# Kernel tuning notes

Measured on AMD Instinct MI355X. Metric: run time of the kernel, lower is better.

## Reference

```python
import jax, jax.numpy as jnp
import numpy as np

B, N, D = 16, 8192, 384   # examples, sentences per example, embedding dim
KN = 16                   # neighbors per node (kNN degree)
K, H, STEPS = 8, 128, 3   # coin dim, hidden dim, walk steps


def setup_inputs() -> dict:
    key = jax.random.key(0)
    ks = jax.random.split(key, 12)
    s = 0.02
    return {
        "sent_embs": jax.random.normal(ks[0], (B, N, D), dtype=jnp.float32),
        "q_embs": jax.random.normal(ks[1], (B, D), dtype=jnp.float32),
        "neighbors": jax.random.randint(ks[2], (B, N, KN), 0, N, dtype=jnp.int32),
        # coin_net: Linear(2D->H), ReLU, Linear(H->K)
        "coin_w1": jax.random.normal(ks[3], (2 * D, H), dtype=jnp.float32) * s,
        "coin_b1": jnp.zeros((H,), dtype=jnp.float32),
        "coin_w2": jax.random.normal(ks[4], (H, K), dtype=jnp.float32) * s,
        "coin_b2": jnp.zeros((K,), dtype=jnp.float32),
        # path_net: Linear(D+K+D->H), ReLU, Linear(H->1)
        "path_w1": jax.random.normal(ks[5], (D + K + D, H), dtype=jnp.float32) * s,
        "path_b1": jnp.zeros((H,), dtype=jnp.float32),
        "path_w2": jax.random.normal(ks[6], (H, 1), dtype=jnp.float32) * s,
        "path_b2": jnp.zeros((1,), dtype=jnp.float32),
    }


def _mlp(x, w1, b1, w2, b2):
    return jax.nn.relu(x @ w1 + b1) @ w2 + b2


def _forward(sent_embs, q_embs, neighbors,
             coin_w1, coin_b1, coin_w2, coin_b2,
             path_w1, path_b1, path_w2, path_b2):
    b, n, d = sent_embs.shape
    k = coin_w2.shape[1]
    q_bcast = jnp.broadcast_to(q_embs[:, None, :], (b, n, d))

    # coin amplitudes per node: [B, N, K]
    amps = _mlp(jnp.concatenate([sent_embs, q_bcast], axis=-1),
                coin_w1, coin_b1, coin_w2, coin_b2)

    # initial uniform walk state: 1/sqrt(N*K)
    state = jnp.full((b, n, k), 1.0 / np.sqrt(n * k), dtype=sent_embs.dtype)

    # adjacency = self-loop + edges row -> neighbors[row]; A @ X == X + masked neighbor gather-sum
    valid = (neighbors >= 0) & (neighbors < n)           # [B, N, KN]
    safe_nbrs = jnp.where(valid, neighbors, 0)
    batch_idx = jnp.arange(b)[:, None, None]

    for _ in range(STEPS):
        ns = state * amps                                # coin step
        gathered = ns[batch_idx, safe_nbrs]              # [B, N, KN, K]
        gathered = jnp.where(valid[..., None], gathered, 0.0)
        ns = ns + gathered.sum(axis=2)                   # sparse.mm(A, ns)
        norm = jnp.linalg.norm(ns.reshape(b, -1), axis=1)[:, None, None]
        state = ns / jnp.where(norm > 0, norm, 1.0)      # renormalize (guard norm==0)

    path_in = jnp.concatenate([sent_embs, state, q_bcast], axis=-1)  # [B, N, D+K+D]
    logits = _mlp(path_in, path_w1, path_b1, path_w2, path_b2)[..., 0]  # [B, N]
    return logits


def reference(sent_embs, q_embs, neighbors,
              coin_w1, coin_b1, coin_w2, coin_b2,
              path_w1, path_b1, path_w2, path_b2):
    return _forward(sent_embs, q_embs, neighbors,
                    coin_w1, coin_b1, coin_w2, coin_b2,
                    path_w1, path_b1, path_w2, path_b2)
```

## Files before the change

kernel.cpp:

```cpp
#include <hip/hip_runtime.h>

#define B_SZ 16
#define N_SZ 8192
#define D_SZ 384
#define KN_SZ 16
#define K_SZ 8
#define H_SZ 128
#define M_TOTAL (B_SZ * N_SZ)
#define KSTEPS 12
#define MT64 (M_TOTAL / 64)
#define CK 128
#define LDSB_STRIDE 144
#define HS_STRIDE 130

typedef short short8 __attribute__((ext_vector_type(8)));
typedef short short4v __attribute__((ext_vector_type(4)));
typedef float floatx4 __attribute__((ext_vector_type(4)));

__device__ __forceinline__ unsigned short f2bf(float f) {
    unsigned u = __builtin_bit_cast(unsigned, f);
    u += 0x7FFFu + ((u >> 16) & 1u);
    return (unsigned short)(u >> 16);
}
__device__ __forceinline__ float bf2f(unsigned short b) {
    unsigned u = ((unsigned)b) << 16;
    return __builtin_bit_cast(float, u);
}
__device__ __forceinline__ unsigned pkbf(float a, float b) {
    unsigned r;
    asm("v_cvt_pk_bf16_f32 %0, %1, %2" : "=v"(r) : "v"(a), "v"(b));
    return r;
}

__global__ void prep_kernel(const float* __restrict__ q_embs,
                            const float* __restrict__ coin_w1,
                            const float* __restrict__ coin_b1,
                            const float* __restrict__ path_w1,
                            const float* __restrict__ path_b1,
                            unsigned short* __restrict__ wswz,
                            float* __restrict__ qcoin, float* __restrict__ qpath,
                            float* __restrict__ norms) {
    int blk = blockIdx.x;
    int t = threadIdx.x;
    if (blk < 384) {
        int f = blk * 256 + t;
        int j  = f & 7;
        int l  = (f >> 3) & 63;
        int ss = (f >> 9) % KSTEPS;
        int ct = f / (KSTEPS * 512);
        int k = ss * 32 + ((l >> 4) << 3) + j;
        int n = ct * 16 + (l & 15);
        float v = (n < H_SZ) ? coin_w1[k * H_SZ + n]
                             : path_w1[k * H_SZ + (n - H_SZ)];
        wswz[f] = f2bf(v);
    } else if (blk == 384) {
        if (t < B_SZ) norms[t] = 0.f;
    } else {
        int b = blk - 385;
        const float* q = q_embs + b * D_SZ;
        if (t < H_SZ) {
            float acc = coin_b1[t];
            for (int d = 0; d < D_SZ; d++)
                acc += q[d] * coin_w1[(D_SZ + d) * H_SZ + t];
            qcoin[b * H_SZ + t] = acc;
        } else if (t < 2 * H_SZ) {
            int h = t - H_SZ;
            float acc = path_b1[h];
            for (int d = 0; d < D_SZ; d++)
                acc += q[d] * path_w1[(D_SZ + K_SZ + d) * H_SZ + h];
            qpath[b * H_SZ + h] = acc;
        }
    }
}

__global__ __launch_bounds__(256)
void gemm_fused(const float* __restrict__ sent,
                const unsigned short* __restrict__ wswz,
                const float* __restrict__ qcoin,
                const float* __restrict__ coin_w2,
                const float* __restrict__ coin_b2,
                unsigned short* __restrict__ hpathB,
                float* __restrict__ amps) {
    __shared__ __align__(16) short als[2 * 64 * LDSB_STRIDE];
    __shared__ float w2s[H_SZ * K_SZ];
    short* buf0 = als;
    short* buf1 = als + 64 * LDSB_STRIDE;
    const int tid = threadIdx.x;
    const int wave = tid >> 6, lane = tid & 63;
    const int m_lane = lane & 15, quad = lane >> 4;
    const int mt = blockIdx.x;
    const int b = mt >> 7;
    const float* abase = sent + (size_t)mt * 64 * D_SZ;
    const int row8 = tid >> 5;
    const int c4   = tid & 31;

    for (int i = tid; i < H_SZ * K_SZ; i += 256) w2s[i] = coin_w2[i];

    const unsigned short* wbase = wswz + (size_t)wave * 4 * KSTEPS * 512 + lane * 8;
    floatx4 acc[4][4];
#pragma unroll
    for (int rt = 0; rt < 4; rt++)
#pragma unroll
        for (int c = 0; c < 4; c++) acc[rt][c] = (floatx4){0.f, 0.f, 0.f, 0.f};

    float4 v[8];

#define STAGE_LOAD(CHUNK)                                                        \
    _Pragma("unroll")                                                            \
    for (int u = 0; u < 8; u++)                                                  \
        v[u] = *(const float4*)(abase + (size_t)(row8 + u * 8) * D_SZ +          \
                                (CHUNK) * CK + c4 * 4);

#define STAGE_STORE(BUF)                                                         \
    _Pragma("unroll")                                                            \
    for (int u = 0; u < 8; u++) {                                                \
        int2 p;                                                                  \
        p.x = (int)pkbf(v[u].x, v[u].y);                                         \
        p.y = (int)pkbf(v[u].z, v[u].w);                                         \
        *(int2*)&(BUF)[(row8 + u * 8) * LDSB_STRIDE + c4 * 4] = p;               \
    }

#define MMA_CHUNK(BUF, CHUNK)                                                    \
    _Pragma("unroll")                                                            \
    for (int sl = 0; sl < 4; sl++) {                                             \
        const int s = (CHUNK) * 4 + sl;                                          \
        short8 bfr[4];                                                           \
        _Pragma("unroll")                                                        \
        for (int cc = 0; cc < 4; cc++)                                           \
            bfr[cc] = *(const short8*)(wbase + (size_t)(cc * KSTEPS + s) * 512); \
        short8 af[4];                                                            \
        _Pragma("unroll")                                                        \
        for (int rt = 0; rt < 4; rt++)                                           \
            af[rt] = *(const short8*)&(BUF)[(rt * 16 + m_lane) * LDSB_STRIDE +   \
                                            sl * 32 + quad * 8];                 \
        _Pragma("unroll")                                                        \
        for (int rt = 0; rt < 4; rt++)                                           \
            _Pragma("unroll")                                                    \
            for (int cc = 0; cc < 4; cc++)                                       \
                acc[rt][cc] = __builtin_amdgcn_mfma_f32_16x16x32_bf16(           \
                    af[rt], bfr[cc], acc[rt][cc], 0, 0, 0);                      \
    }

    STAGE_LOAD(0);
    STAGE_STORE(buf0);
    __syncthreads();
    STAGE_LOAD(1);
    MMA_CHUNK(buf0, 0);
    STAGE_STORE(buf1);
    __syncthreads();
    STAGE_LOAD(2);
    MMA_CHUNK(buf1, 1);
    STAGE_STORE(buf0);
    __syncthreads();
    MMA_CHUNK(buf0, 2);

    if (wave >= 2) {
        const int colw = (wave & 1) * 64;
#pragma unroll
        for (int rt = 0; rt < 4; rt++) {
            int mt16 = mt * 4 + rt;
#pragma unroll
            for (int c = 0; c < 4; c++) {
                int col = colw + c * 16 + m_lane;
                int2 p;
                p.x = (int)pkbf(acc[rt][c][0], acc[rt][c][1]);
                p.y = (int)pkbf(acc[rt][c][2], acc[rt][c][3]);
                *(int2*)(hpathB + (size_t)mt16 * 2048 + col * 16 + quad * 4) = p;
            }
        }
    }
    __syncthreads();

    float* hs = (float*)als;
    if (wave < 2) {
        const int colw = wave * 64;
        float qc[4];
#pragma unroll
        for (int c = 0; c < 4; c++)
            qc[c] = qcoin[b * H_SZ + colw + c * 16 + m_lane];
#pragma unroll
        for (int rt = 0; rt < 4; rt++)
#pragma unroll
            for (int c = 0; c < 4; c++) {
                int colj = colw + c * 16 + m_lane;
#pragma unroll
                for (int j = 0; j < 4; j++) {
                    int row = rt * 16 + quad * 4 + j;
                    float hv = acc[rt][c][j] + qc[c];
                    hs[row * HS_STRIDE + colj] = hv > 0.f ? hv : 0.f;
                }
            }
    }
    __syncthreads();

    {
        const int r = tid >> 2;
        const int kk = (tid & 3) * 2;
        float a0 = coin_b2[kk], a1 = coin_b2[kk + 1];
#pragma unroll 8
        for (int c = 0; c < H_SZ; c++) {
            float hv = hs[r * HS_STRIDE + c];
            float2 w = *(const float2*)&w2s[c * 8 + kk];
            a0 += hv * w.x; a1 += hv * w.y;
        }
        const size_t m = (size_t)mt * 64 + r;
        *(float2*)(amps + m * 8 + kk) = make_float2(a0, a1);
    }
#undef STAGE_LOAD
#undef STAGE_STORE
#undef MMA_CHUNK
}

__global__ __launch_bounds__(1024)
void walk_fused(const float* __restrict__ amps,
                const int* __restrict__ neighbors,
                float* __restrict__ zfinal,
                float* __restrict__ norms) {
    __shared__ float z0buf[N_SZ];
    __shared__ float z1buf[N_SZ];
    __shared__ float bsum;
    const int tid = threadIdx.x;
    const int b = blockIdx.x >> 3;
    const int k = blockIdx.x & 7;
    const size_t nodebase = (size_t)b * N_SZ;

    float a[8];
#pragma unroll
    for (int u = 0; u < 8; u++) {
        int n = u * 1024 + tid;
        a[u] = amps[(nodebase + n) * 8 + k];
        z0buf[n] = a[u] * (1.0f / 256.0f);
    }
    if (tid == 0) bsum = 0.f;
    __syncthreads();

    float* zc = z0buf;
    float* zn = z1buf;
    float ss = 0.f;
#pragma unroll
    for (int step = 0; step < 3; step++) {
#pragma unroll
        for (int u = 0; u < 8; u++) {
            const int n = u * 1024 + tid;
            const int4* nb4 = (const int4*)(neighbors + (nodebase + n) * KN_SZ);
            int4 q0 = nb4[0], q1 = nb4[1], q2 = nb4[2], q3 = nb4[3];
            float v = zc[n];
            int idx[16] = {q0.x, q0.y, q0.z, q0.w, q1.x, q1.y, q1.z, q1.w,
                           q2.x, q2.y, q2.z, q2.w, q3.x, q3.y, q3.z, q3.w};
#pragma unroll
            for (int i = 0; i < 16; i++) {
                int nn = idx[i];
                if ((unsigned)nn < (unsigned)N_SZ) v += zc[nn];
            }
            if (step < 2) v *= a[u];
            zn[n] = v;
            if (step == 2) ss += v * v;
        }
        __syncthreads();
        float* t = zc; zc = zn; zn = t;
    }

#pragma unroll
    for (int o = 32; o > 0; o >>= 1) ss += __shfl_down(ss, o);
    if ((tid & 63) == 0) atomicAdd(&bsum, ss);
    __syncthreads();
    if (tid == 0) atomicAdd(&norms[b], bsum);

#pragma unroll
    for (int u = 0; u < 8; u++) {
        int n = u * 1024 + tid;
        zfinal[(nodebase + n) * 8 + k] = zc[n];
    }
}

__global__ __launch_bounds__(256)
void logits_kernel(const unsigned short* __restrict__ hpathB,
                   const float* __restrict__ qpath,
                   const float* __restrict__ u2,
                   const float* __restrict__ norms,
                   const float* __restrict__ path_w1,
                   const float* __restrict__ path_w2,
                   const float* __restrict__ path_b2,
                   float* __restrict__ out) {
    __shared__ float w1t[4 * 260];
    __shared__ float w2sp[4 * 33];
    __shared__ float qps[4 * 33];
    const int tid = threadIdx.x;
    const int mbase = blockIdx.x * 64;
    const int b = mbase >> 13;
    for (int i2 = tid; i2 < H_SZ * K_SZ; i2 += 256) {
        int h = i2 >> 3, j = i2 & 7;
        w1t[(h >> 5) * 260 + (h & 31) * 8 + j] = path_w1[(D_SZ + j) * H_SZ + h];
    }
    if (tid < H_SZ) {
        int idx = (tid >> 5) * 33 + (tid & 31);
        w2sp[idx] = path_w2[tid];
        qps[idx]  = qpath[b * H_SZ + tid];
    }
    __syncthreads();

    const int m = mbase + (tid >> 2);
    const int seg = tid & 3;
    float ssq = norms[b];
    float inv = ssq > 0.f ? rsqrtf(ssq) : 1.0f;
    float st[K_SZ];
    {
        float4 s0 = *(const float4*)(u2 + (size_t)m * 8);
        float4 s1 = *(const float4*)(u2 + (size_t)m * 8 + 4);
        st[0] = s0.x * inv; st[1] = s0.y * inv; st[2] = s0.z * inv; st[3] = s0.w * inv;
        st[4] = s1.x * inv; st[5] = s1.y * inv; st[6] = s1.z * inv; st[7] = s1.w * inv;
    }
    const unsigned short* hb = hpathB + (size_t)(m >> 4) * 2048 + (m & 15);
    const float* w1b = &w1t[seg * 260];
    const float* w2b = &w2sp[seg * 33];
    const float* qpb = &qps[seg * 33];
    const int hseg = seg * 32;

    float acc = 0.f;
#pragma unroll 8
    for (int i = 0; i < 32; i++) {
        float hv = bf2f(hb[(hseg + i) * 16]) + qpb[i];
        float4 wa = *(const float4*)&w1b[i * 8];
        float4 wb = *(const float4*)&w1b[i * 8 + 4];
        hv += st[0]*wa.x + st[1]*wa.y + st[2]*wa.z + st[3]*wa.w
            + st[4]*wb.x + st[5]*wb.y + st[6]*wb.z + st[7]*wb.w;
        hv = hv > 0.f ? hv : 0.f;
        acc += hv * w2b[i];
    }
    acc += __shfl_xor(acc, 1);
    acc += __shfl_xor(acc, 2);
    if (seg == 0) out[m] = acc + path_b2[0];
}

extern "C" void kernel_launch(void* const* d_in, const int* in_sizes, int n_in,
                              void* d_out, int out_size, void* d_ws, size_t ws_size,
                              hipStream_t stream) {
    const float* sent      = (const float*)d_in[0];
    const float* q_embs    = (const float*)d_in[1];
    const int*   neighbors = (const int*)d_in[2];
    const float* coin_w1   = (const float*)d_in[3];
    const float* coin_b1   = (const float*)d_in[4];
    const float* coin_w2   = (const float*)d_in[5];
    const float* coin_b2   = (const float*)d_in[6];
    const float* path_w1   = (const float*)d_in[7];
    const float* path_b1   = (const float*)d_in[8];
    const float* path_w2   = (const float*)d_in[9];
    const float* path_b2   = (const float*)d_in[10];
    float* out = (float*)d_out;

    char* ws = (char*)d_ws;
    unsigned short* wswz = (unsigned short*)ws;
    float* qcoin = (float*)(ws + 196608);
    float* qpath = (float*)(ws + 204800);
    float* norms = (float*)(ws + 212992);
    unsigned short* hpathB = (unsigned short*)(ws + 213248);
    float* amps = (float*)(ws + 33767680);
    float* zB   = (float*)(ws + 37961984);

    prep_kernel<<<401, 256, 0, stream>>>(q_embs, coin_w1, coin_b1, path_w1, path_b1,
                                         wswz, qcoin, qpath, norms);
    gemm_fused<<<MT64, 256, 0, stream>>>(sent, wswz, qcoin, coin_w2, coin_b2,
                                         hpathB, amps);
    walk_fused<<<B_SZ * K_SZ, 1024, 0, stream>>>(amps, neighbors, zB, norms);
    logits_kernel<<<M_TOTAL / 64, 256, 0, stream>>>(hpathB, qpath, zB, norms,
                                                    path_w1, path_w2, path_b2, out);
}
```

Baseline: 393.8 us.

## Load GEMM A operand directly from global into registers, drop LDS staging

```diff
diff --git a/kernel.cpp b/kernel.cpp
--- a/kernel.cpp
+++ b/kernel.cpp
@@ -9,12 +9,9 @@
 #define M_TOTAL (B_SZ * N_SZ)
 #define KSTEPS 12
 #define MT64 (M_TOTAL / 64)
-#define CK 128
-#define LDSB_STRIDE 144
 #define HS_STRIDE 130
 
 typedef short short8 __attribute__((ext_vector_type(8)));
-typedef short short4v __attribute__((ext_vector_type(4)));
 typedef float floatx4 __attribute__((ext_vector_type(4)));
 
 __device__ __forceinline__ unsigned short f2bf(float f) {
@@ -30,6 +27,14 @@
     unsigned r;
     asm("v_cvt_pk_bf16_f32 %0, %1, %2" : "=v"(r) : "v"(a), "v"(b));
     return r;
+}
+__device__ __forceinline__ short8 cvt8(float4 lo, float4 hi) {
+    union { int4 i; short8 s; } u;
+    u.i.x = (int)pkbf(lo.x, lo.y);
+    u.i.y = (int)pkbf(lo.z, lo.w);
+    u.i.z = (int)pkbf(hi.x, hi.y);
+    u.i.w = (int)pkbf(hi.z, hi.w);
+    return u.s;
 }
 
 __global__ void prep_kernel(const float* __restrict__ q_embs,
@@ -81,78 +86,53 @@
                 const float* __restrict__ coin_b2,
                 unsigned short* __restrict__ hpathB,
                 float* __restrict__ amps) {
-    __shared__ __align__(16) short als[2 * 64 * LDSB_STRIDE];
+    __shared__ float hs[64 * HS_STRIDE];
     __shared__ float w2s[H_SZ * K_SZ];
-    short* buf0 = als;
-    short* buf1 = als + 64 * LDSB_STRIDE;
     const int tid = threadIdx.x;
     const int wave = tid >> 6, lane = tid & 63;
     const int m_lane = lane & 15, quad = lane >> 4;
     const int mt = blockIdx.x;
     const int b = mt >> 7;
-    const float* abase = sent + (size_t)mt * 64 * D_SZ;
-    const int row8 = tid >> 5;
-    const int c4   = tid & 31;
 
     for (int i = tid; i < H_SZ * K_SZ; i += 256) w2s[i] = coin_w2[i];
 
+    const float* aF = sent + (size_t)mt * 64 * D_SZ + (size_t)m_lane * D_SZ + quad * 8;
     const unsigned short* wbase = wswz + (size_t)wave * 4 * KSTEPS * 512 + lane * 8;
+
     floatx4 acc[4][4];
 #pragma unroll
     for (int rt = 0; rt < 4; rt++)
 #pragma unroll
         for (int c = 0; c < 4; c++) acc[rt][c] = (floatx4){0.f, 0.f, 0.f, 0.f};
 
-    float4 v[8];
-
-#define STAGE_LOAD(CHUNK)                                                        \
+    float4 ca[4], cb[4];
+#define LOADA(S)                                                                 \
     _Pragma("unroll")                                                            \
-    for (int u = 0; u < 8; u++)                                                  \
-        v[u] = *(const float4*)(abase + (size_t)(row8 + u * 8) * D_SZ +          \
-                                (CHUNK) * CK + c4 * 4);
-
-#define STAGE_STORE(BUF)                                                         \
-    _Pragma("unroll")                                                            \
-    for (int u = 0; u < 8; u++) {                                                \
-        int2 p;                                                                  \
-        p.x = (int)pkbf(v[u].x, v[u].y);                                         \
-        p.y = (int)pkbf(v[u].z, v[u].w);                                         \
-        *(int2*)&(BUF)[(row8 + u * 8) * LDSB_STRIDE + c4 * 4] = p;               \
-    }
-
-#define MMA_CHUNK(BUF, CHUNK)                                                    \
-    _Pragma("unroll")                                                            \
-    for (int sl = 0; sl < 4; sl++) {                                             \
-        const int s = (CHUNK) * 4 + sl;                                          \
-        short8 bfr[4];                                                           \
-        _Pragma("unroll")                                                        \
-        for (int cc = 0; cc < 4; cc++)                                           \
-            bfr[cc] = *(const short8*)(wbase + (size_t)(cc * KSTEPS + s) * 512); \
-        short8 af[4];                                                            \
-        _Pragma("unroll")                                                        \
-        for (int rt = 0; rt < 4; rt++)                                           \
-            af[rt] = *(const short8*)&(BUF)[(rt * 16 + m_lane) * LDSB_STRIDE +   \
-                                            sl * 32 + quad * 8];                 \
-        _Pragma("unroll")                                                        \
-        for (int rt = 0; rt < 4; rt++)                                           \
-            _Pragma("unroll")                                                    \
-            for (int cc = 0; cc < 4; cc++)                                       \
-                acc[rt][cc] = __builtin_amdgcn_mfma_f32_16x16x32_bf16(           \
-                    af[rt], bfr[cc], acc[rt][cc], 0, 0, 0);                      \
-    }
-
-    STAGE_LOAD(0);
-    STAGE_STORE(buf0);
-    __syncthreads();
-    STAGE_LOAD(1);
-    MMA_CHUNK(buf0, 0);
-    STAGE_STORE(buf1);
-    __syncthreads();
-    STAGE_LOAD(2);
-    MMA_CHUNK(buf1, 1);
-    STAGE_STORE(buf0);
-    __syncthreads();
-    MMA_CHUNK(buf0, 2);
+    for (int rt = 0; rt < 4; rt++) {                                             \
+        const float* p = aF + (size_t)rt * 16 * D_SZ + (S) * 32;                 \
+        ca[rt] = *(const float4*)p;                                              \
+        cb[rt] = *(const float4*)(p + 4);                                        \
+    }
+
+    LOADA(0);
+#pragma unroll 1
+    for (int s = 0; s < KSTEPS; s++) {
+        short8 bfr[4];
+#pragma unroll
+        for (int cc = 0; cc < 4; cc++)
+            bfr[cc] = *(const short8*)(wbase + (size_t)(cc * KSTEPS + s) * 512);
+        short8 af[4];
+#pragma unroll
+        for (int rt = 0; rt < 4; rt++) af[rt] = cvt8(ca[rt], cb[rt]);
+        if (s + 1 < KSTEPS) { LOADA(s + 1); }
+#pragma unroll
+        for (int rt = 0; rt < 4; rt++)
+#pragma unroll
+            for (int cc = 0; cc < 4; cc++)
+                acc[rt][cc] = __builtin_amdgcn_mfma_f32_16x16x32_bf16(
+                    af[rt], bfr[cc], acc[rt][cc], 0, 0, 0);
+    }
+#undef LOADA
 
     if (wave >= 2) {
         const int colw = (wave & 1) * 64;
@@ -169,9 +149,7 @@
             }
         }
     }
-    __syncthreads();
-
-    float* hs = (float*)als;
+
     if (wave < 2) {
         const int colw = wave * 64;
         float qc[4];
@@ -206,9 +184,6 @@
         const size_t m = (size_t)mt * 64 + r;
         *(float2*)(amps + m * 8 + kk) = make_float2(a0, a1);
     }
-#undef STAGE_LOAD
-#undef STAGE_STORE
-#undef MMA_CHUNK
 }
 
 __global__ __launch_bounds__(1024)
```

After: 426.8 us. 1.08x slower.

## Process two row tiles per GEMM block with cross-tile prefetch and vectorized coin epilogue

Applied to the files above, without the earlier changes.

```diff
diff --git a/kernel.cpp b/kernel.cpp
--- a/kernel.cpp
+++ b/kernel.cpp
@@ -14,8 +14,8 @@
 #define HS_STRIDE 130
 
 typedef short short8 __attribute__((ext_vector_type(8)));
-typedef short short4v __attribute__((ext_vector_type(4)));
 typedef float floatx4 __attribute__((ext_vector_type(4)));
+typedef float f32x4 __attribute__((ext_vector_type(4)));
 
 __device__ __forceinline__ unsigned short f2bf(float f) {
     unsigned u = __builtin_bit_cast(unsigned, f);
@@ -82,15 +82,16 @@
                 unsigned short* __restrict__ hpathB,
                 float* __restrict__ amps) {
     __shared__ __align__(16) short als[2 * 64 * LDSB_STRIDE];
-    __shared__ float w2s[H_SZ * K_SZ];
+    __shared__ __align__(16) float w2s[H_SZ * K_SZ];
     short* buf0 = als;
     short* buf1 = als + 64 * LDSB_STRIDE;
     const int tid = threadIdx.x;
     const int wave = tid >> 6, lane = tid & 63;
     const int m_lane = lane & 15, quad = lane >> 4;
-    const int mt = blockIdx.x;
-    const int b = mt >> 7;
-    const float* abase = sent + (size_t)mt * 64 * D_SZ;
+    const int mt0 = blockIdx.x * 2;
+    const int b = mt0 >> 7;
+    const float* a0 = sent + (size_t)mt0 * 64 * D_SZ;
+    const float* a1 = a0 + 64 * D_SZ;
     const int row8 = tid >> 5;
     const int c4   = tid & 31;
 
@@ -98,18 +99,21 @@
 
     const unsigned short* wbase = wswz + (size_t)wave * 4 * KSTEPS * 512 + lane * 8;
     floatx4 acc[4][4];
-#pragma unroll
-    for (int rt = 0; rt < 4; rt++)
-#pragma unroll
+    f32x4 v[8];
+    float* hs = (float*)als;
+
+#define ZERO_ACC()                                                               \
+    _Pragma("unroll")                                                            \
+    for (int rt = 0; rt < 4; rt++)                                               \
+        _Pragma("unroll")                                                        \
         for (int c = 0; c < 4; c++) acc[rt][c] = (floatx4){0.f, 0.f, 0.f, 0.f};
 
-    float4 v[8];
-
-#define STAGE_LOAD(CHUNK)                                                        \
+#define STAGE_LOAD(AB, CHUNK)                                                    \
     _Pragma("unroll")                                                            \
     for (int u = 0; u < 8; u++)                                                  \
-        v[u] = *(const float4*)(abase + (size_t)(row8 + u * 8) * D_SZ +          \
-                                (CHUNK) * CK + c4 * 4);
+        v[u] = __builtin_nontemporal_load(                                       \
+            (const f32x4*)((AB) + (size_t)(row8 + u * 8) * D_SZ +                \
+                           (CHUNK) * CK + c4 * 4));
 
 #define STAGE_STORE(BUF)                                                         \
     _Pragma("unroll")                                                            \
@@ -141,74 +145,95 @@
                     af[rt], bfr[cc], acc[rt][cc], 0, 0, 0);                      \
     }
 
-    STAGE_LOAD(0);
+#define EPILOGUE(MT)                                                             \
+    do {                                                                         \
+        if (wave >= 2) {                                                         \
+            const int colw = (wave & 1) * 64;                                    \
+            _Pragma("unroll")                                                    \
+            for (int rt = 0; rt < 4; rt++) {                                     \
+                int mt16 = (MT) * 4 + rt;                                        \
+                _Pragma("unroll")                                                \
+                for (int c = 0; c < 4; c++) {                                    \
+                    int col = colw + c * 16 + m_lane;                            \
+                    int2 p;                                                      \
+                    p.x = (int)pkbf(acc[rt][c][0], acc[rt][c][1]);               \
+                    p.y = (int)pkbf(acc[rt][c][2], acc[rt][c][3]);               \
+                    *(int2*)(hpathB + (size_t)mt16 * 2048 + col * 16 +           \
+                             quad * 4) = p;                                      \
+                }                                                                \
+            }                                                                    \
+        }                                                                        \
+        __syncthreads();                              \
+        if (wave < 2) {                                                          \
+            const int colw = wave * 64;                                          \
+            float qc[4];                                                         \
+            _Pragma("unroll")                                                    \
+            for (int c = 0; c < 4; c++)                                          \
+                qc[c] = qcoin[b * H_SZ + colw + c * 16 + m_lane];                \
+            _Pragma("unroll")                                                    \
+            for (int rt = 0; rt < 4; rt++)                                       \
+                _Pragma("unroll")                                                \
+                for (int c = 0; c < 4; c++) {                                    \
+                    int colj = colw + c * 16 + m_lane;                           \
+                    _Pragma("unroll")                                            \
+                    for (int j = 0; j < 4; j++) {                                \
+                        int row = rt * 16 + quad * 4 + j;                        \
+                        float hv = acc[rt][c][j] + qc[c];                        \
+                        hs[row * HS_STRIDE + colj] = hv > 0.f ? hv : 0.f;        \
+                    }                                                            \
+                }                                                                \
+        }                                                                        \
+        __syncthreads();                                                         \
+        {                                                                        \
+            const int r  = tid >> 2;                                             \
+            const int kp = (tid >> 1) & 1;                                       \
+            const int hf = tid & 1;                                              \
+            float4 a4 = (hf == 0) ? *(const float4*)(coin_b2 + kp * 4)           \
+                                  : make_float4(0.f, 0.f, 0.f, 0.f);             \
+            const float* hrow = hs + r * HS_STRIDE + hf * 64;                    \
+            const float* wb   = w2s + hf * 512 + kp * 4;                         \
+            _Pragma("unroll 16")                                                 \
+            for (int c = 0; c < 64; c++) {                                       \
+                float hv = hrow[c];                                              \
+                float4 w = *(const float4*)(wb + c * 8);                         \
+                a4.x += hv * w.x; a4.y += hv * w.y;                              \
+                a4.z += hv * w.z; a4.w += hv * w.w;                              \
+            }                                                                    \
+            a4.x += __shfl_xor(a4.x, 1);                                         \
+            a4.y += __shfl_xor(a4.y, 1);                                         \
+            a4.z += __shfl_xor(a4.z, 1);                                         \
+            a4.w += __shfl_xor(a4.w, 1);                                         \
+            if (hf == 0) {                                                       \
+                const size_t m = (size_t)(MT) * 64 + r;                          \
+                *(float4*)(amps + m * 8 + kp * 4) = a4;                          \
+            }                                                                    \
+        }                                                                        \
+    } while (0)
+
+    ZERO_ACC();
+    STAGE_LOAD(a0, 0);
     STAGE_STORE(buf0);
     __syncthreads();
-    STAGE_LOAD(1);
-    MMA_CHUNK(buf0, 0);
-    STAGE_STORE(buf1);
-    __syncthreads();
-    STAGE_LOAD(2);
-    MMA_CHUNK(buf1, 1);
+    STAGE_LOAD(a0, 1);  MMA_CHUNK(buf0, 0);  STAGE_STORE(buf1);  __syncthreads();
+    STAGE_LOAD(a0, 2);  MMA_CHUNK(buf1, 1);  STAGE_STORE(buf0);  __syncthreads();
+    STAGE_LOAD(a1, 0);
+    MMA_CHUNK(buf0, 2);
+    EPILOGUE(mt0);
+    __syncthreads();
+
+    ZERO_ACC();
     STAGE_STORE(buf0);
     __syncthreads();
+    STAGE_LOAD(a1, 1);  MMA_CHUNK(buf0, 0);  STAGE_STORE(buf1);  __syncthreads();
+    STAGE_LOAD(a1, 2);  MMA_CHUNK(buf1, 1);  STAGE_STORE(buf0);  __syncthreads();
     MMA_CHUNK(buf0, 2);
-
-    if (wave >= 2) {
-        const int colw = (wave & 1) * 64;
-#pragma unroll
-        for (int rt = 0; rt < 4; rt++) {
-            int mt16 = mt * 4 + rt;
-#pragma unroll
-            for (int c = 0; c < 4; c++) {
-                int col = colw + c * 16 + m_lane;
-                int2 p;
-                p.x = (int)pkbf(acc[rt][c][0], acc[rt][c][1]);
-                p.y = (int)pkbf(acc[rt][c][2], acc[rt][c][3]);
-                *(int2*)(hpathB + (size_t)mt16 * 2048 + col * 16 + quad * 4) = p;
-            }
-        }
-    }
-    __syncthreads();
-
-    float* hs = (float*)als;
-    if (wave < 2) {
-        const int colw = wave * 64;
-        float qc[4];
-#pragma unroll
-        for (int c = 0; c < 4; c++)
-            qc[c] = qcoin[b * H_SZ + colw + c * 16 + m_lane];
-#pragma unroll
-        for (int rt = 0; rt < 4; rt++)
-#pragma unroll
-            for (int c = 0; c < 4; c++) {
-                int colj = colw + c * 16 + m_lane;
-#pragma unroll
-                for (int j = 0; j < 4; j++) {
-                    int row = rt * 16 + quad * 4 + j;
-                    float hv = acc[rt][c][j] + qc[c];
-                    hs[row * HS_STRIDE + colj] = hv > 0.f ? hv : 0.f;
-                }
-            }
-    }
-    __syncthreads();
-
-    {
-        const int r = tid >> 2;
-        const int kk = (tid & 3) * 2;
-        float a0 = coin_b2[kk], a1 = coin_b2[kk + 1];
-#pragma unroll 8
-        for (int c = 0; c < H_SZ; c++) {
-            float hv = hs[r * HS_STRIDE + c];
-            float2 w = *(const float2*)&w2s[c * 8 + kk];
-            a0 += hv * w.x; a1 += hv * w.y;
-        }
-        const size_t m = (size_t)mt * 64 + r;
-        *(float2*)(amps + m * 8 + kk) = make_float2(a0, a1);
-    }
+    EPILOGUE(mt0 + 1);
+
+#undef ZERO_ACC
 #undef STAGE_LOAD
 #undef STAGE_STORE
 #undef MMA_CHUNK
+#undef EPILOGUE
 }
 
 __global__ __launch_bounds__(1024)
@@ -359,8 +384,8 @@
 
     prep_kernel<<<401, 256, 0, stream>>>(q_embs, coin_w1, coin_b1, path_w1, path_b1,
                                          wswz, qcoin, qpath, norms);
-    gemm_fused<<<MT64, 256, 0, stream>>>(sent, wswz, qcoin, coin_w2, coin_b2,
-                                         hpathB, amps);
+    gemm_fused<<<MT64 / 2, 256, 0, stream>>>(sent, wswz, qcoin, coin_w2, coin_b2,
+                                             hpathB, amps);
     walk_fused<<<B_SZ * K_SZ, 1024, 0, stream>>>(amps, neighbors, zB, norms);
     logits_kernel<<<M_TOTAL / 64, 256, 0, stream>>>(hpathB, qpath, zB, norms,
                                                     path_w1, path_w2, path_b2, out);
```

Result: slower. 410.9 us (+4.4%).
